# Performance work log

Hardware: AMD Instinct MI355X
Metric: run time of the kernel (lower is better)

Reference implementation:

```python
import jax, jax.numpy as jnp
import numpy as np

B, S, D = 2, 2048, 1024
N_HEADS, D_HEAD = 16, 64
INIT_STD = 0.02


def setup_inputs() -> dict:
    key = jax.random.key(0)
    k_res, k_q, k_k, k_v, k_o = jax.random.split(key, 5)
    residual = jax.random.normal(k_res, (B, S, D), dtype=jnp.float32)
    W_Q = INIT_STD * jax.random.normal(k_q, (N_HEADS, D_HEAD, D), dtype=jnp.float32)
    W_K = INIT_STD * jax.random.normal(k_k, (N_HEADS, D_HEAD, D), dtype=jnp.float32)
    W_V = INIT_STD * jax.random.normal(k_v, (N_HEADS, D_HEAD, D), dtype=jnp.float32)
    W_O = INIT_STD * jax.random.normal(k_o, (N_HEADS, D_HEAD, D), dtype=jnp.float32)
    return {"residual": residual, "W_Q": W_Q, "W_K": W_K, "W_V": W_V, "W_O": W_O}


def reference(residual, W_Q, W_K, W_V, W_O):
    seq_len = residual.shape[1]
    # projections: [b, n, p, h]  (heads first, matching q.transpose(1,2))
    q = jnp.einsum('bpd,nhd->bnph', residual, W_Q)
    k = jnp.einsum('bpd,nhd->bnph', residual, W_K)
    v = jnp.einsum('bpd,nhd->bnph', residual, W_V)
    scale = 1.0 / jnp.sqrt(jnp.asarray(q.shape[-1], dtype=residual.dtype))
    # [b, n, p_q, p_k] full score matrix (faithful to original naive impl)
    scores = jnp.einsum('bnqh,bnkh->bnqk', q, k) * scale
    causal = jnp.tril(jnp.ones((seq_len, seq_len), dtype=bool))
    scores = jnp.where(causal, scores, -jnp.inf)
    pattern = jax.nn.softmax(scores, axis=-1)
    attn_out = jnp.einsum('bnqk,bnkh->bnqh', pattern, v)
    # output projection summed over heads: 'bpnh,nhd->bpd'
    return jnp.einsum('bnph,nhd->bpd', attn_out, W_O)
```

## Files before the change

### kernel.cpp

```cpp
#include <hip/hip_runtime.h>
#include <math.h>


#define SS_ 2048
#define DD_ 1024
#define NH_ 16
#define BN_ 32
#define BS_ 4096

typedef __bf16 bf16x8 __attribute__((ext_vector_type(8)));
typedef __bf16 bf16x4 __attribute__((ext_vector_type(4)));
typedef short shortx4 __attribute__((ext_vector_type(4)));
typedef float floatx4 __attribute__((ext_vector_type(4)));
typedef unsigned short ushortx4 __attribute__((ext_vector_type(4)));

__device__ __forceinline__ unsigned short f2bf(float f) {
    union { float f; unsigned u; } v; v.f = f;
    unsigned r = v.u + 0x7FFFu + ((v.u >> 16) & 1u);
    return (unsigned short)(r >> 16);
}

__device__ __forceinline__ floatx4 mfma_pv(bf16x4 a, bf16x4 b, floatx4 c) {
#if __has_builtin(__builtin_amdgcn_mfma_f32_16x16x16_bf16)
    return __builtin_amdgcn_mfma_f32_16x16x16_bf16(a, b, c, 0, 0, 0);
#else
    return __builtin_amdgcn_mfma_f32_16x16x16bf16_1k(
        __builtin_bit_cast(shortx4, a), __builtin_bit_cast(shortx4, b), c, 0, 0, 0);
#endif
}

__device__ __forceinline__ void gl_lds16(const unsigned short* g, unsigned short* l) {
    __builtin_amdgcn_global_load_lds(
        (const __attribute__((address_space(1))) unsigned int*)g,
        (__attribute__((address_space(3))) unsigned int*)l, 16, 0, 0);
}

__global__ __launch_bounds__(256) void cast_bf16_kernel(
    const float* __restrict__ resid, const float* __restrict__ WQ,
    const float* __restrict__ WK, const float* __restrict__ WV,
    unsigned short* __restrict__ residB, unsigned short* __restrict__ WQb,
    unsigned short* __restrict__ WKb, unsigned short* __restrict__ WVb)
{
    const int z = blockIdx.y;
    if (z > 0 && blockIdx.x >= 1024) return;
    const float* src = (z == 0) ? resid : (z == 1) ? WQ : (z == 2) ? WK : WV;
    unsigned short* dst = (z == 0) ? residB : (z == 1) ? WQb : (z == 2) ? WKb : WVb;
    const int i = (blockIdx.x * 256 + threadIdx.x) * 4;
    float4 f = *(const float4*)(src + i);
    ushortx4 o;
    o[0] = f2bf(f.x); o[1] = f2bf(f.y); o[2] = f2bf(f.z); o[3] = f2bf(f.w);
    *(ushortx4*)(dst + i) = o;
}

__global__ __launch_bounds__(256) void wo_transpose_kernel(
    const float* __restrict__ WO, unsigned short* __restrict__ WOt)
{
    __shared__ float t[64][65];
    const int kk0 = blockIdx.x * 64, d0 = blockIdx.y * 64;
    #pragma unroll
    for (int it = 0; it < 16; ++it) {
        int idx = it * 256 + threadIdx.x;
        int r = idx >> 6, c = idx & 63;
        t[r][c] = WO[(kk0 + r) * DD_ + d0 + c];
    }
    __syncthreads();
    #pragma unroll
    for (int it = 0; it < 16; ++it) {
        int idx = it * 256 + threadIdx.x;
        int r = idx >> 6, c = idx & 63;
        WOt[(d0 + r) * DD_ + kk0 + c] = f2bf(t[c][r]);
    }
}

__global__ __launch_bounds__(256) void qkv_m97_kernel(
    const unsigned short* __restrict__ residB,
    const unsigned short* __restrict__ WQb,
    const unsigned short* __restrict__ WKb,
    const unsigned short* __restrict__ WVb,
    unsigned short* __restrict__ q, unsigned short* __restrict__ kk,
    unsigned short* __restrict__ vT)
{
    __shared__ unsigned short As[128 * 64];
    __shared__ unsigned short Bs[128 * 64];
    const int tid = threadIdx.x;
    const int l = tid & 63, w = tid >> 6;
    const int quad = l >> 4, lan = l & 15;
    const int z = blockIdx.z;
    const unsigned short* W = (z == 0) ? WQb : (z == 1) ? WKb : WVb;
    unsigned short* dst = (z == 0) ? q : (z == 1) ? kk : vT;
    const int mBase = blockIdx.x * 128;
    const int nBase = blockIdx.y * 128;
    const int wm = (w & 1) * 64, wn = (w >> 1) * 64;

    floatx4 acc[4][4];
    #pragma unroll
    for (int a = 0; a < 4; ++a)
        #pragma unroll
        for (int b = 0; b < 4; ++b)
            #pragma unroll
            for (int i = 0; i < 4; ++i) acc[a][b][i] = 0.f;

    const int sr = l >> 3;
    const int sgx = ((l & 7) ^ sr) * 8;

    for (int k0 = 0; k0 < DD_; k0 += 64) {
        __syncthreads();
        #pragma unroll
        for (int i = 0; i < 4; ++i) {
            const int row = i * 32 + w * 8 + sr;
            gl_lds16(residB + (size_t)(mBase + row) * DD_ + k0 + sgx,
                     As + i * 2048 + w * 512);
            gl_lds16(W + (size_t)(nBase + row) * DD_ + k0 + sgx,
                     Bs + i * 2048 + w * 512);
        }
        __syncthreads();
        #pragma unroll
        for (int ks = 0; ks < 2; ++ks) {
            const int fo = (((ks * 4 + quad) ^ (lan & 7)) << 3);
            bf16x8 a[4], b[4];
            #pragma unroll
            for (int mi = 0; mi < 4; ++mi)
                a[mi] = *(const bf16x8*)(As + (wm + mi * 16 + lan) * 64 + fo);
            #pragma unroll
            for (int ni = 0; ni < 4; ++ni)
                b[ni] = *(const bf16x8*)(Bs + (wn + ni * 16 + lan) * 64 + fo);
            #pragma unroll
            for (int mi = 0; mi < 4; ++mi)
                #pragma unroll
                for (int ni = 0; ni < 4; ++ni)
                    acc[mi][ni] = __builtin_amdgcn_mfma_f32_16x16x32_bf16(
                        a[mi], b[ni], acc[mi][ni], 0, 0, 0);
        }
    }
    const int headU = (nBase + wn) >> 6;
    const float scale = (z == 0) ? 0.125f * 1.44269504088896340736f : 1.0f;
    if (z < 2) {
        #pragma unroll
        for (int mi = 0; mi < 4; ++mi)
            #pragma unroll
            for (int ni = 0; ni < 4; ++ni)
                #pragma unroll
                for (int reg = 0; reg < 4; ++reg) {
                    int m = mBase + wm + mi * 16 + quad * 4 + reg;
                    int bb = m >> 11, ss = m & 2047;
                    int h = ni * 16 + lan;
                    dst[((size_t)(bb * NH_ + headU) * SS_ + ss) * 64 + h] =
                        f2bf(acc[mi][ni][reg] * scale);
                }
    } else {
        #pragma unroll
        for (int mi = 0; mi < 4; ++mi) {
            const int m0 = mBase + wm + mi * 16 + quad * 4;
            const int bb = m0 >> 11, ss0 = m0 & 2047;
            #pragma unroll
            for (int ni = 0; ni < 4; ++ni) {
                const int h = ni * 16 + lan;
                bf16x4 ob;
                #pragma unroll
                for (int reg = 0; reg < 4; ++reg)
                    ob[reg] = static_cast<__bf16>(acc[mi][ni][reg]);
                *(bf16x4*)(dst + ((size_t)(bb * NH_ + headU) * 64 + h) * SS_ + ss0) = ob;
            }
        }
    }
}

__global__ __launch_bounds__(256) void flash_mfma_kernel(
    const unsigned short* __restrict__ q,
    const unsigned short* __restrict__ k,
    const unsigned short* __restrict__ vT,
    unsigned short* __restrict__ attn)
{
    __shared__ unsigned short ldsK[2][64 * 64];
    __shared__ unsigned short ldsV[2][64 * 64];
    const int l = threadIdx.x & 63, w = threadIdx.x >> 6;
    const int quad = l >> 4, lan = l & 15;
    const int f = blockIdx.x;
    const int bn = (f & 7) | (((f >> 3) & 3) << 3);
    const int chunk = 31 - (f >> 5);

    const unsigned short* Qg = q  + (size_t)bn * SS_ * 64;
    const unsigned short* Kg = k  + (size_t)bn * SS_ * 64;
    const unsigned short* Vg = vT + (size_t)bn * 64 * SS_;

    const int srl = l >> 3;
    const int sgx = (l & 7) ^ srl;

    const int qRow0 = chunk * 64 + w * 16;
    const int qAbs = qRow0 + lan;

    const unsigned short* Qr = Qg + (size_t)qAbs * 64 + quad * 8;
    bf16x8 Qf0 = *(const bf16x8*)(Qr);
    bf16x8 Qf1 = *(const bf16x8*)(Qr + 32);

    bf16x4 ones;
    #pragma unroll
    for (int i = 0; i < 4; ++i) ones[i] = static_cast<__bf16>(1.0f);

    float mrow = -INFINITY;
    floatx4 l_acc;
    floatx4 o[4];
    #pragma unroll
    for (int i = 0; i < 4; ++i) l_acc[i] = 0.f;
    #pragma unroll
    for (int t = 0; t < 4; ++t)
        #pragma unroll
        for (int i = 0; i < 4; ++i) o[t][i] = 0.f;

    #pragma unroll
    for (int i = 0; i < 2; ++i) {
        const int row = w * 16 + i * 8;
        gl_lds16(Kg + (size_t)(row + srl) * 64 + sgx * 8, &ldsK[0][row * 64]);
        gl_lds16(Vg + (size_t)(row + srl) * SS_ + sgx * 8, &ldsV[0][row * 64]);
    }

    for (int kt = 0; kt <= chunk; ++kt) {
        const int kBase = kt * 64;
        const int buf = kt & 1;
        __syncthreads();
        if (kt < chunk) {
            const int kB1 = kBase + 64;
            #pragma unroll
            for (int i = 0; i < 2; ++i) {
                const int row = w * 16 + i * 8;
                gl_lds16(Kg + (size_t)(kB1 + row + srl) * 64 + sgx * 8,
                         &ldsK[buf ^ 1][row * 64]);
                gl_lds16(Vg + (size_t)(row + srl) * SS_ + kB1 + sgx * 8,
                         &ldsV[buf ^ 1][row * 64]);
            }
        }
        const unsigned short* Kb = &ldsK[buf][0];
        const unsigned short* Vb = &ldsV[buf][0];

        floatx4 sc[4];
        #pragma unroll
        for (int nt = 0; nt < 4; ++nt) {
            const unsigned short* kr = Kb + (nt * 16 + lan) * 64;
            bf16x8 K0 = *(const bf16x8*)(kr + ((quad ^ (lan & 7)) << 3));
            bf16x8 K1 = *(const bf16x8*)(kr + (((quad + 4) ^ (lan & 7)) << 3));
            floatx4 zz; zz[0] = zz[1] = zz[2] = zz[3] = 0.f;
            sc[nt] = __builtin_amdgcn_mfma_f32_16x16x32_bf16(K0, Qf0, zz, 0, 0, 0);
            sc[nt] = __builtin_amdgcn_mfma_f32_16x16x32_bf16(K1, Qf1, sc[nt], 0, 0, 0);
        }
        if (kt == chunk) {
            #pragma unroll
            for (int nt = 0; nt < 4; ++nt)
                #pragma unroll
                for (int reg = 0; reg < 4; ++reg)
                    if (kBase + nt * 16 + quad * 4 + reg > qAbs)
                        sc[nt][reg] = -INFINITY;
        }
        float mx = sc[0][0];
        #pragma unroll
        for (int nt = 0; nt < 4; ++nt)
            #pragma unroll
            for (int reg = 0; reg < 4; ++reg) mx = fmaxf(mx, sc[nt][reg]);
        mx = fmaxf(mx, __shfl_xor(mx, 16, 64));
        mx = fmaxf(mx, __shfl_xor(mx, 32, 64));
        const float mnew = fmaxf(mrow, mx);
        const float alpha = exp2f(mrow - mnew);
        mrow = mnew;
        bf16x4 pb[4];
        #pragma unroll
        for (int nt = 0; nt < 4; ++nt)
            #pragma unroll
            for (int reg = 0; reg < 4; ++reg)
                pb[nt][reg] = static_cast<__bf16>(exp2f(sc[nt][reg] - mnew));
        l_acc[0] *= alpha;
        #pragma unroll
        for (int t = 0; t < 4; ++t)
            #pragma unroll
            for (int i = 0; i < 4; ++i) o[t][i] *= alpha;
        #pragma unroll
        for (int nt = 0; nt < 4; ++nt)
            l_acc = mfma_pv(ones, pb[nt], l_acc);
        #pragma unroll
        for (int t = 0; t < 4; ++t) {
            const unsigned short* vr = Vb + (t * 16 + lan) * 64 + ((quad & 1) << 2);
            #pragma unroll
            for (int nt = 0; nt < 4; ++nt) {
                const int g = nt * 2 + (quad >> 1);
                bf16x4 Vf = *(const bf16x4*)(vr + ((g ^ (lan & 7)) << 3));
                o[t] = mfma_pv(Vf, pb[nt], o[t]);
            }
        }
    }
    const float rl = 1.f / l_acc[0];
    #pragma unroll
    for (int t = 0; t < 4; ++t) {
        bf16x4 ob;
        #pragma unroll
        for (int reg = 0; reg < 4; ++reg)
            ob[reg] = static_cast<__bf16>(o[t][reg] * rl);
        *(bf16x4*)(attn + ((size_t)bn * SS_ + qAbs) * 64 + t * 16 + quad * 4) = ob;
    }
}

__global__ __launch_bounds__(256) void out_m97_kernel(
    const unsigned short* __restrict__ attn,
    const unsigned short* __restrict__ WOt,
    float* __restrict__ out)
{
    __shared__ unsigned short As[128 * 64];
    __shared__ unsigned short Bs[128 * 64];
    const int tid = threadIdx.x;
    const int l = tid & 63, w = tid >> 6;
    const int quad = l >> 4, lan = l & 15;
    const int mBase = blockIdx.x * 128;
    const int nBase = blockIdx.y * 128;
    const int wm = (w & 1) * 64, wn = (w >> 1) * 64;
    const int bbU = mBase >> 11;
    const int ssBase = mBase & 2047;

    floatx4 acc[4][4];
    #pragma unroll
    for (int a = 0; a < 4; ++a)
        #pragma unroll
        for (int b = 0; b < 4; ++b)
            #pragma unroll
            for (int i = 0; i < 4; ++i) acc[a][b][i] = 0.f;

    const int sr = l >> 3;
    const int sgx = ((l & 7) ^ sr) * 8;

    for (int kt = 0; kt < 16; ++kt) {
        const int k0 = kt * 64;
        __syncthreads();
        #pragma unroll
        for (int i = 0; i < 4; ++i) {
            const int row = i * 32 + w * 8 + sr;
            gl_lds16(attn + ((size_t)(bbU * NH_ + kt) * SS_ + ssBase + row) * 64 + sgx,
                     As + i * 2048 + w * 512);
            gl_lds16(WOt + (size_t)(nBase + row) * DD_ + k0 + sgx,
                     Bs + i * 2048 + w * 512);
        }
        __syncthreads();
        #pragma unroll
        for (int ks = 0; ks < 2; ++ks) {
            const int fo = (((ks * 4 + quad) ^ (lan & 7)) << 3);
            bf16x8 a[4], b[4];
            #pragma unroll
            for (int mi = 0; mi < 4; ++mi)
                a[mi] = *(const bf16x8*)(As + (wm + mi * 16 + lan) * 64 + fo);
            #pragma unroll
            for (int ni = 0; ni < 4; ++ni)
                b[ni] = *(const bf16x8*)(Bs + (wn + ni * 16 + lan) * 64 + fo);
            #pragma unroll
            for (int mi = 0; mi < 4; ++mi)
                #pragma unroll
                for (int ni = 0; ni < 4; ++ni)
                    acc[mi][ni] = __builtin_amdgcn_mfma_f32_16x16x32_bf16(
                        a[mi], b[ni], acc[mi][ni], 0, 0, 0);
        }
    }
    #pragma unroll
    for (int mi = 0; mi < 4; ++mi)
        #pragma unroll
        for (int ni = 0; ni < 4; ++ni)
            #pragma unroll
            for (int reg = 0; reg < 4; ++reg) {
                int m = mBase + wm + mi * 16 + quad * 4 + reg;
                out[(size_t)m * DD_ + nBase + wn + ni * 16 + lan] = acc[mi][ni][reg];
            }
}

extern "C" void kernel_launch(void* const* d_in, const int* in_sizes, int n_in,
                              void* d_out, int out_size, void* d_ws, size_t ws_size,
                              hipStream_t stream) {
    const float* resid = (const float*)d_in[0];
    const float* WQ    = (const float*)d_in[1];
    const float* WK    = (const float*)d_in[2];
    const float* WV    = (const float*)d_in[3];
    const float* WO    = (const float*)d_in[4];
    float* out = (float*)d_out;

    unsigned short* q      = (unsigned short*)d_ws;
    unsigned short* kk     = q      + 4194304;
    unsigned short* vT     = kk     + 4194304;
    unsigned short* attn   = vT     + 4194304;
    unsigned short* residB = attn   + 4194304;
    unsigned short* WQb    = residB + 4194304;
    unsigned short* WKb    = WQb    + 1048576;
    unsigned short* WVb    = WKb    + 1048576;
    unsigned short* WOt    = WVb    + 1048576;

    cast_bf16_kernel<<<dim3(4096, 4), 256, 0, stream>>>(
        resid, WQ, WK, WV, residB, WQb, WKb, WVb);
    wo_transpose_kernel<<<dim3(16, 16), 256, 0, stream>>>(WO, WOt);
    qkv_m97_kernel<<<dim3(32, 8, 3), 256, 0, stream>>>(
        residB, WQb, WKb, WVb, q, kk, vT);
    flash_mfma_kernel<<<dim3(1024), dim3(256), 0, stream>>>(q, kk, vT, attn);
    out_m97_kernel<<<dim3(32, 8), 256, 0, stream>>>(attn, WOt, out);
}
```

Measured before the change: 196.7 us.

## Software-pipeline QK scores one tile ahead with triple-buffered K in flash kernel

The flash attention loop now computes the QK^T scores for the next key tile while the softmax and PV for the current tile run. K is triple-buffered in LDS and staged two tiles ahead, while V stays double-buffered and is staged one tile ahead. The online-softmax rescale of the output and running sum is skipped when no row max in the wave increased. Launch bounds now request 4 waves per SIMD. The extra score registers and the occupancy hint may cause register pressure or spills.

```diff
diff --git a/kernel.cpp b/kernel.cpp
--- a/kernel.cpp
+++ b/kernel.cpp
@@ -165,13 +165,13 @@
     }
 }
 
-__global__ __launch_bounds__(256) void flash_mfma_kernel(
+__global__ __launch_bounds__(256, 4) void flash_mfma_kernel(
     const unsigned short* __restrict__ q,
     const unsigned short* __restrict__ k,
     const unsigned short* __restrict__ vT,
     unsigned short* __restrict__ attn)
 {
-    __shared__ unsigned short ldsK[2][64 * 64];
+    __shared__ unsigned short ldsK[3][64 * 64];
     __shared__ unsigned short ldsV[2][64 * 64];
     const int l = threadIdx.x & 63, w = threadIdx.x >> 6;
     const int quad = l >> 4, lan = l & 15;
@@ -207,40 +207,43 @@
         #pragma unroll
         for (int i = 0; i < 4; ++i) o[t][i] = 0.f;
 
-    #pragma unroll
-    for (int i = 0; i < 2; ++i) {
-        const int row = w * 16 + i * 8;
-        gl_lds16(Kg + (size_t)(row + srl) * 64 + sgx * 8, &ldsK[0][row * 64]);
-        gl_lds16(Vg + (size_t)(row + srl) * SS_ + sgx * 8, &ldsV[0][row * 64]);
-    }
+    #define STAGE_K(kt_, buf_)                                                  \
+        { const int row0_ = w * 16, kB_ = (kt_) * 64;                           \
+          gl_lds16(Kg + (size_t)(kB_ + row0_ + srl) * 64 + sgx * 8,             \
+                   &ldsK[buf_][row0_ * 64]);                                    \
+          gl_lds16(Kg + (size_t)(kB_ + row0_ + 8 + srl) * 64 + sgx * 8,         \
+                   &ldsK[buf_][(row0_ + 8) * 64]); }
+    #define STAGE_V(kt_, buf_)                                                  \
+        { const int row0_ = w * 16, kB_ = (kt_) * 64;                           \
+          gl_lds16(Vg + (size_t)(row0_ + srl) * SS_ + kB_ + sgx * 8,            \
+                   &ldsV[buf_][row0_ * 64]);                                    \
+          gl_lds16(Vg + (size_t)(row0_ + 8 + srl) * SS_ + kB_ + sgx * 8,        \
+                   &ldsV[buf_][(row0_ + 8) * 64]); }
+    #define QK_TILE(dst_, buf_)                                                 \
+        { const unsigned short* Kb_ = &ldsK[buf_][0];                           \
+          _Pragma("unroll")                                                     \
+          for (int nt = 0; nt < 4; ++nt) {                                      \
+              const unsigned short* kr_ = Kb_ + (nt * 16 + lan) * 64;           \
+              bf16x8 K0_ = *(const bf16x8*)(kr_ + ((quad ^ (lan & 7)) << 3));   \
+              bf16x8 K1_ = *(const bf16x8*)(kr_ + (((quad + 4) ^ (lan & 7)) << 3)); \
+              floatx4 zz_; zz_[0] = zz_[1] = zz_[2] = zz_[3] = 0.f;             \
+              dst_[nt] = __builtin_amdgcn_mfma_f32_16x16x32_bf16(K0_, Qf0, zz_, 0, 0, 0); \
+              dst_[nt] = __builtin_amdgcn_mfma_f32_16x16x32_bf16(K1_, Qf1, dst_[nt], 0, 0, 0); } }
+
+    STAGE_K(0, 0);
+    STAGE_V(0, 0);
+    __syncthreads();
+    if (chunk >= 1) STAGE_K(1, 1);
+    floatx4 scCur[4], scNext[4];
+    QK_TILE(scCur, 0);
 
     for (int kt = 0; kt <= chunk; ++kt) {
         const int kBase = kt * 64;
-        const int buf = kt & 1;
         __syncthreads();
-        if (kt < chunk) {
-            const int kB1 = kBase + 64;
-            #pragma unroll
-            for (int i = 0; i < 2; ++i) {
-                const int row = w * 16 + i * 8;
-                gl_lds16(Kg + (size_t)(kB1 + row + srl) * 64 + sgx * 8,
-                         &ldsK[buf ^ 1][row * 64]);
-                gl_lds16(Vg + (size_t)(row + srl) * SS_ + kB1 + sgx * 8,
-                         &ldsV[buf ^ 1][row * 64]);
-            }
-        }
-        const unsigned short* Kb = &ldsK[buf][0];
-        const unsigned short* Vb = &ldsV[buf][0];
-
-        floatx4 sc[4];
-        #pragma unroll
-        for (int nt = 0; nt < 4; ++nt) {
-            const unsigned short* kr = Kb + (nt * 16 + lan) * 64;
-            bf16x8 K0 = *(const bf16x8*)(kr + ((quad ^ (lan & 7)) << 3));
-            bf16x8 K1 = *(const bf16x8*)(kr + (((quad + 4) ^ (lan & 7)) << 3));
-            floatx4 zz; zz[0] = zz[1] = zz[2] = zz[3] = 0.f;
-            sc[nt] = __builtin_amdgcn_mfma_f32_16x16x32_bf16(K0, Qf0, zz, 0, 0, 0);
-            sc[nt] = __builtin_amdgcn_mfma_f32_16x16x32_bf16(K1, Qf1, sc[nt], 0, 0, 0);
+        if (kt + 2 <= chunk) STAGE_K(kt + 2, (kt + 2) % 3);
+        if (kt + 1 <= chunk) {
+            STAGE_V(kt + 1, (kt + 1) & 1);
+            QK_TILE(scNext, (kt + 1) % 3);
         }
         if (kt == chunk) {
             #pragma unroll
@@ -248,32 +251,35 @@
                 #pragma unroll
                 for (int reg = 0; reg < 4; ++reg)
                     if (kBase + nt * 16 + quad * 4 + reg > qAbs)
-                        sc[nt][reg] = -INFINITY;
-        }
-        float mx = sc[0][0];
+                        scCur[nt][reg] = -INFINITY;
+        }
+        float mx = scCur[0][0];
         #pragma unroll
         for (int nt = 0; nt < 4; ++nt)
             #pragma unroll
-            for (int reg = 0; reg < 4; ++reg) mx = fmaxf(mx, sc[nt][reg]);
+            for (int reg = 0; reg < 4; ++reg) mx = fmaxf(mx, scCur[nt][reg]);
         mx = fmaxf(mx, __shfl_xor(mx, 16, 64));
         mx = fmaxf(mx, __shfl_xor(mx, 32, 64));
         const float mnew = fmaxf(mrow, mx);
-        const float alpha = exp2f(mrow - mnew);
+        if (!__all(mx <= mrow)) {
+            const float alpha = exp2f(mrow - mnew);
+            l_acc[0] *= alpha;
+            #pragma unroll
+            for (int t = 0; t < 4; ++t)
+                #pragma unroll
+                for (int i = 0; i < 4; ++i) o[t][i] *= alpha;
+        }
         mrow = mnew;
         bf16x4 pb[4];
         #pragma unroll
         for (int nt = 0; nt < 4; ++nt)
             #pragma unroll
             for (int reg = 0; reg < 4; ++reg)
-                pb[nt][reg] = static_cast<__bf16>(exp2f(sc[nt][reg] - mnew));
-        l_acc[0] *= alpha;
-        #pragma unroll
-        for (int t = 0; t < 4; ++t)
-            #pragma unroll
-            for (int i = 0; i < 4; ++i) o[t][i] *= alpha;
+                pb[nt][reg] = static_cast<__bf16>(exp2f(scCur[nt][reg] - mnew));
         #pragma unroll
         for (int nt = 0; nt < 4; ++nt)
             l_acc = mfma_pv(ones, pb[nt], l_acc);
+        const unsigned short* Vb = &ldsV[kt & 1][0];
         #pragma unroll
         for (int t = 0; t < 4; ++t) {
             const unsigned short* vr = Vb + (t * 16 + lan) * 64 + ((quad & 1) << 2);
@@ -284,6 +290,8 @@
                 o[t] = mfma_pv(Vf, pb[nt], o[t]);
             }
         }
+        #pragma unroll
+        for (int nt = 0; nt < 4; ++nt) scCur[nt] = scNext[nt];
     }
     const float rl = 1.f / l_acc[0];
     #pragma unroll
@@ -294,6 +302,9 @@
             ob[reg] = static_cast<__bf16>(o[t][reg] * rl);
         *(bf16x4*)(attn + ((size_t)bn * SS_ + qAbs) * 64 + t * 16 + quad * 4) = ob;
     }
+    #undef STAGE_K
+    #undef STAGE_V
+    #undef QK_TILE
 }
 
 __global__ __launch_bounds__(256) void out_m97_kernel(
```

Result: no change. 193.7 us (-1.5%).
